# Optimization experiments

Measured on AMD Instinct MI355X. Metric: run time of the kernel, lower is better.

Reference implementation:

```python
import jax, jax.numpy as jnp
import numpy as np

EMBED_DIM = 1024
NUM_HEADS = 16
HEAD_DIM = EMBED_DIM // NUM_HEADS
B, N = 4, 2048


def setup_inputs() -> dict:
    key = jax.random.key(0)
    k = jax.random.split(key, 5)
    scale = 1.0 / np.sqrt(EMBED_DIM)
    return {
        "x": jax.random.normal(k[0], (B, N, EMBED_DIM), dtype=jnp.float32),
        # torch nn.Linear convention: y = x @ W.T + b, W shape [out, in]
        "qkv_w": jax.random.uniform(k[1], (3 * EMBED_DIM, EMBED_DIM), jnp.float32, -scale, scale),
        "qkv_b": jax.random.uniform(k[2], (3 * EMBED_DIM,), jnp.float32, -scale, scale),
        "out_w": jax.random.uniform(k[3], (EMBED_DIM, EMBED_DIM), jnp.float32, -scale, scale),
        "out_b": jax.random.uniform(k[4], (EMBED_DIM,), jnp.float32, -scale, scale),
    }


def reference(x, qkv_w, qkv_b, out_w, out_b):
    b, n, e = x.shape
    qkv = x @ qkv_w.T + qkv_b                      # [B,N,3E]
    qkv = qkv.reshape(b, n, 3, NUM_HEADS, HEAD_DIM)
    qkv = jnp.transpose(qkv, (2, 0, 3, 1, 4))      # [3,B,H,N,D]
    q, k, v = qkv[0], qkv[1], qkv[2]
    scores = jnp.einsum("bhqd,bhkd->bhqk", q, k) / np.sqrt(HEAD_DIM)
    weights = jax.nn.softmax(scores, axis=-1)
    attn = jnp.einsum("bhqk,bhkd->bhqd", weights, v)  # [B,H,N,D]
    attn = jnp.transpose(attn, (0, 2, 1, 3)).reshape(b, n, e)
    return attn @ out_w.T + out_b
```

## Files before the change

### kernel.cpp

```cpp
#include <hip/hip_runtime.h>
#include <hip/hip_bf16.h>

#define EMBED 1024
#define NHEADS 16
#define HDIM 64
#define BATCH 4
#define SEQ 2048
#define MROWS (BATCH*SEQ)
#define QKVN (3*EMBED)
#define KDIM 1024

typedef __bf16 bf16;
typedef __bf16 bf16x4 __attribute__((ext_vector_type(4)));
typedef __bf16 bf16x8 __attribute__((ext_vector_type(8)));
typedef float f32x4 __attribute__((ext_vector_type(4)));
typedef float f32x16 __attribute__((ext_vector_type(16)));

#define QSCALE 0.18033688011112042f

#define NX (MROWS*EMBED/4)
#define NQ (QKVN*KDIM/4)
#define NO (EMBED*KDIM/4)
__global__ void cvt_all(const float* __restrict__ x, const float* __restrict__ qw,
                        const float* __restrict__ ow,
                        bf16* __restrict__ xb, bf16* __restrict__ qwb, bf16* __restrict__ owb) {
    int i = blockIdx.x * blockDim.x + threadIdx.x;
    const float* src; bf16* dst; int j;
    if (i < NX)            { src = x;  dst = xb;  j = i; }
    else if (i < NX + NQ)  { src = qw; dst = qwb; j = i - NX; }
    else if (i < NX+NQ+NO) { src = ow; dst = owb; j = i - NX - NQ; }
    else return;
    float4 f = ((const float4*)src)[j];
    bf16x4 o;
    o[0] = (bf16)f.x; o[1] = (bf16)f.y; o[2] = (bf16)f.z; o[3] = (bf16)f.w;
    *((bf16x4*)dst + j) = o;
}

template<int MODE>
__launch_bounds__(256)
__global__ void gemm_bt(const bf16* __restrict__ A, const bf16* __restrict__ B,
                        const float* __restrict__ bias,
                        float* __restrict__ outF,
                        bf16* __restrict__ Qb, bf16* __restrict__ Kb, bf16* __restrict__ Vt)
{
    __shared__ bf16 Alds[128][32];
    __shared__ bf16 Blds[128][32];
    const int tid = threadIdx.x;
    const int l = tid & 63, w = tid >> 6;
    const int wr = w >> 1, wc = w & 1;
    const int tM = blockIdx.y * 128, tN = blockIdx.x * 128;

    f32x4 acc[4][4] = {};
    const bf16* Abase = A + (size_t)tM * KDIM;
    const bf16* Bbase = B + (size_t)tN * KDIM;

    for (int k0 = 0; k0 < KDIM; k0 += 32) {
        #pragma unroll
        for (int t = 0; t < 2; ++t) {
            int idx = t * 256 + tid;
            int row = idx >> 2;
            int kc = (idx & 3) * 8;
            __builtin_amdgcn_global_load_lds(
                (const __attribute__((address_space(1))) void*)(Abase + (size_t)row * KDIM + k0 + kc),
                (__attribute__((address_space(3))) void*)((char*)&Alds[0][0] + idx * 16),
                16, 0, 0);
            __builtin_amdgcn_global_load_lds(
                (const __attribute__((address_space(1))) void*)(Bbase + (size_t)row * KDIM + k0 + kc),
                (__attribute__((address_space(3))) void*)((char*)&Blds[0][0] + idx * 16),
                16, 0, 0);
        }
        __syncthreads();
        bf16x8 a[4], b[4];
        #pragma unroll
        for (int i = 0; i < 4; ++i)
            a[i] = *(const bf16x8*)&Alds[wr * 64 + i * 16 + (l & 15)][(l >> 4) * 8];
        #pragma unroll
        for (int j = 0; j < 4; ++j)
            b[j] = *(const bf16x8*)&Blds[wc * 64 + j * 16 + (l & 15)][(l >> 4) * 8];
        #pragma unroll
        for (int i = 0; i < 4; ++i)
            #pragma unroll
            for (int j = 0; j < 4; ++j)
                acc[i][j] = __builtin_amdgcn_mfma_f32_16x16x32_bf16(a[i], b[j], acc[i][j], 0, 0, 0);
        __syncthreads();
    }

    #pragma unroll
    for (int i = 0; i < 4; ++i) {
        #pragma unroll
        for (int j = 0; j < 4; ++j) {
            int n = tN + wc * 64 + j * 16 + (l & 15);
            float bv = bias[n];
            #pragma unroll
            for (int r = 0; r < 4; ++r) {
                int m = tM + wr * 64 + i * 16 + (l >> 4) * 4 + r;
                float v = acc[i][j][r] + bv;
                if (MODE == 1) {
                    outF[(size_t)m * EMBED + n] = v;
                } else {
                    int which = n >> 10, nn = n & 1023;
                    int hd = nn >> 6, d = nn & 63;
                    int bidx = m >> 11, ns = m & 2047;
                    int bh = bidx * NHEADS + hd;
                    int t32 = ns >> 5;
                    if (which == 2) {
                        int rem16 = ns & 15;
                        int c = (ns >> 4) & 1;
                        int fj = (rem16 & 3) | ((rem16 & 8) >> 1);
                        int fhi = (rem16 >> 2) & 1;
                        int dblk = d >> 5;
                        int lane = (d & 31) | (fhi << 5);
                        size_t idx = ((((size_t)bh * 64 + t32) * 2 + dblk) * 2 + c) * 512 + lane * 8 + fj;
                        Vt[idx] = (bf16)v;
                    } else {
                        int kk = d >> 4, fhi = (d >> 3) & 1, fj = d & 7;
                        int lane = (ns & 31) | (fhi << 5);
                        size_t idx = (((size_t)bh * 64 + t32) * 4 + kk) * 512 + lane * 8 + fj;
                        if (which == 0) Qb[idx] = (bf16)(v * QSCALE);
                        else            Kb[idx] = (bf16)v;
                    }
                }
            }
        }
    }
}

static __device__ __forceinline__ unsigned cvt_pk(float lo, float hi) {
    unsigned r;
    asm("v_cvt_pk_bf16_f32 %0, %1, %2" : "=v"(r) : "v"(lo), "v"(hi));
    return r;
}

__launch_bounds__(256)
__global__ void attn_kernel(const bf16* __restrict__ Qb, const bf16* __restrict__ Kb,
                            const bf16* __restrict__ Vt, bf16* __restrict__ AO)
{
    const int tid = threadIdx.x, l = tid & 63, w = tid >> 6;
    const int lo5 = l & 31, hi = l >> 5;
    int bid = blockIdx.x;
    int swz = (bid & 7) * 128 + (bid >> 3);
    const int bh = swz >> 4;
    const int qt = swz & 15;

    const bf16* QFh = Qb + (size_t)bh * (64 * 2048);
    const bf16* Kit = Kb + (size_t)bh * (64 * 2048) + (size_t)l * 8;
    const bf16* Vit = Vt + (size_t)bh * (64 * 2048) + (size_t)l * 8;

    const int qtile = qt * 4 + w;
    const bf16* qbase = QFh + (size_t)qtile * 2048 + (size_t)l * 8;
    bf16x8 qf[4];
    #pragma unroll
    for (int kk = 0; kk < 4; ++kk)
        qf[kk] = *(const bf16x8*)(qbase + kk * 512);

    f32x16 O0 = {}, O1 = {};
    float lsum = 0.f;

    bf16x8 kK0, kK1, kK2, kK3;
    kK0 = *(const bf16x8*)(Kit);
    kK1 = *(const bf16x8*)(Kit + 512);
    kK2 = *(const bf16x8*)(Kit + 1024);
    kK3 = *(const bf16x8*)(Kit + 1536);
    f32x16 SA, SB;
    #pragma unroll
    for (int r = 0; r < 16; ++r) SA[r] = 0.f;
    SA = __builtin_amdgcn_mfma_f32_32x32x16_bf16(kK0, qf[0], SA, 0, 0, 0);
    SA = __builtin_amdgcn_mfma_f32_32x32x16_bf16(kK1, qf[1], SA, 0, 0, 0);
    SA = __builtin_amdgcn_mfma_f32_32x32x16_bf16(kK2, qf[2], SA, 0, 0, 0);
    SA = __builtin_amdgcn_mfma_f32_32x32x16_bf16(kK3, qf[3], SA, 0, 0, 0);
    kK0 = *(const bf16x8*)(Kit + 2048);
    kK1 = *(const bf16x8*)(Kit + 2048 + 512);
    kK2 = *(const bf16x8*)(Kit + 2048 + 1024);
    kK3 = *(const bf16x8*)(Kit + 2048 + 1536);

#define ATTN_BODY(T, SCUR, SNXT)                                                        \
    {                                                                                    \
        const int t = (T);                                                               \
        const bf16* vb = Vit + (size_t)t * 2048;                                         \
        bf16x8 vf00 = *(const bf16x8*)(vb);                                              \
        bf16x8 vf01 = *(const bf16x8*)(vb + 512);                                        \
        bf16x8 vf10 = *(const bf16x8*)(vb + 1024);                                       \
        bf16x8 vf11 = *(const bf16x8*)(vb + 1536);                                       \
        __builtin_amdgcn_s_setprio(1);                                                   \
        _Pragma("unroll")                                                                \
        for (int r = 0; r < 16; ++r) SNXT[r] = 0.f;                                      \
        SNXT = __builtin_amdgcn_mfma_f32_32x32x16_bf16(kK0, qf[0], SNXT, 0, 0, 0);       \
        SNXT = __builtin_amdgcn_mfma_f32_32x32x16_bf16(kK1, qf[1], SNXT, 0, 0, 0);       \
        SNXT = __builtin_amdgcn_mfma_f32_32x32x16_bf16(kK2, qf[2], SNXT, 0, 0, 0);       \
        SNXT = __builtin_amdgcn_mfma_f32_32x32x16_bf16(kK3, qf[3], SNXT, 0, 0, 0);       \
        __builtin_amdgcn_s_setprio(0);                                                   \
        int tp = t + 2; tp = (tp < 64) ? tp : 0;                                         \
        const bf16* kb = Kit + (size_t)tp * 2048;                                        \
        kK0 = *(const bf16x8*)(kb);                                                      \
        kK1 = *(const bf16x8*)(kb + 512);                                                \
        kK2 = *(const bf16x8*)(kb + 1024);                                               \
        kK3 = *(const bf16x8*)(kb + 1536);                                               \
        float p[16];                                                                     \
        _Pragma("unroll")                                                                \
        for (int r = 0; r < 16; ++r)                                                     \
            p[r] = __builtin_amdgcn_exp2f(SCUR[r]);                                      \
        float s0 = (p[0] + p[1]) + (p[2] + p[3]);                                        \
        float s1 = (p[4] + p[5]) + (p[6] + p[7]);                                        \
        float s2 = (p[8] + p[9]) + (p[10] + p[11]);                                      \
        float s3 = (p[12] + p[13]) + (p[14] + p[15]);                                    \
        lsum += (s0 + s1) + (s2 + s3);                                                   \
        union { unsigned u[4]; bf16x8 v; } pk0, pk1;                                     \
        pk0.u[0] = cvt_pk(p[0], p[1]);   pk0.u[1] = cvt_pk(p[2], p[3]);                  \
        pk0.u[2] = cvt_pk(p[4], p[5]);   pk0.u[3] = cvt_pk(p[6], p[7]);                  \
        pk1.u[0] = cvt_pk(p[8], p[9]);   pk1.u[1] = cvt_pk(p[10], p[11]);                \
        pk1.u[2] = cvt_pk(p[12], p[13]); pk1.u[3] = cvt_pk(p[14], p[15]);                \
        __builtin_amdgcn_s_setprio(1);                                                   \
        O0 = __builtin_amdgcn_mfma_f32_32x32x16_bf16(vf00, pk0.v, O0, 0, 0, 0);          \
        O0 = __builtin_amdgcn_mfma_f32_32x32x16_bf16(vf01, pk1.v, O0, 0, 0, 0);          \
        O1 = __builtin_amdgcn_mfma_f32_32x32x16_bf16(vf10, pk0.v, O1, 0, 0, 0);          \
        O1 = __builtin_amdgcn_mfma_f32_32x32x16_bf16(vf11, pk1.v, O1, 0, 0, 0);          \
        __builtin_amdgcn_s_setprio(0);                                                   \
    }

    for (int t2 = 0; t2 < 64; t2 += 2) {
        ATTN_BODY(t2,     SA, SB)
        ATTN_BODY(t2 + 1, SB, SA)
    }
#undef ATTN_BODY

    lsum += __shfl_xor(lsum, 32);
    float linv = 1.0f / lsum;

    const int b = bh >> 4, hd = bh & 15;
    const int q0 = qt * 128 + w * 32;
    bf16* outp = &AO[(size_t)(b * SEQ + q0 + lo5) * EMBED + hd * HDIM];
    #pragma unroll
    for (int g = 0; g < 4; ++g) {
        bf16x4 o0, o1;
        #pragma unroll
        for (int r4 = 0; r4 < 4; ++r4) {
            o0[r4] = (bf16)(O0[g * 4 + r4] * linv);
            o1[r4] = (bf16)(O1[g * 4 + r4] * linv);
        }
        *(bf16x4*)&outp[g * 8 + hi * 4] = o0;
        *(bf16x4*)&outp[32 + g * 8 + hi * 4] = o1;
    }
}

extern "C" void kernel_launch(void* const* d_in, const int* in_sizes, int n_in,
                              void* d_out, int out_size, void* d_ws, size_t ws_size,
                              hipStream_t stream) {
    const float* x     = (const float*)d_in[0];
    const float* qkv_w = (const float*)d_in[1];
    const float* qkv_b = (const float*)d_in[2];
    const float* out_w = (const float*)d_in[3];
    const float* out_b = (const float*)d_in[4];
    float* out = (float*)d_out;

    char* ws = (char*)d_ws;
    bf16* xb  = (bf16*)(ws);
    bf16* qwb = (bf16*)(ws + 16777216);
    bf16* owb = (bf16*)(ws + 23068672);
    bf16* Qb  = (bf16*)(ws + 25165824);
    bf16* Kb  = (bf16*)(ws + 41943040);
    bf16* Vt  = (bf16*)(ws + 58720256);
    bf16* AO  = (bf16*)(ws + 75497472);

    cvt_all<<<(NX + NQ + NO + 255) / 256, 256, 0, stream>>>(x, qkv_w, out_w, xb, qwb, owb);

    gemm_bt<0><<<dim3(QKVN / 128, MROWS / 128), 256, 0, stream>>>(
        xb, qwb, qkv_b, nullptr, Qb, Kb, Vt);

    attn_kernel<<<BATCH * NHEADS * (SEQ / 128), 256, 0, stream>>>(Qb, Kb, Vt, AO);

    gemm_bt<1><<<dim3(EMBED / 128, MROWS / 128), 256, 0, stream>>>(
        AO, owb, out_b, out, nullptr, nullptr, nullptr);
}
```

Baseline: 201.7 us.

## Stage QKV epilogue through LDS for coalesced stores and prefetch V a tile ahead

The QKV GEMM epilogue used to scatter single bf16 values straight to global memory in the attention fragment layout. It now writes the biased, scaled values into an LDS bounce buffer that reuses the GEMM tile space, in two passes, then copies them out as contiguous 16-byte stores. The attention kernel now also double-buffers V fragments in registers, loading the next tile's V one iteration early so the load latency overlaps the current compute. The costs are extra barriers and LDS traffic in the epilogue and more registers in the attention loop, which could lower occupancy.

New measurement: 200.7 us. Within noise of the previous version (-0.5%).

```diff
diff --git a/kernel.cpp b/kernel.cpp
--- a/kernel.cpp
+++ b/kernel.cpp
@@ -43,8 +43,11 @@
                         float* __restrict__ outF,
                         bf16* __restrict__ Qb, bf16* __restrict__ Kb, bf16* __restrict__ Vt)
 {
-    __shared__ bf16 Alds[128][32];
-    __shared__ bf16 Blds[128][32];
+    __shared__ __align__(16) char ldsmem[16384];
+    bf16 (*Alds)[32] = (bf16(*)[32])ldsmem;
+    bf16 (*Blds)[32] = (bf16(*)[32])(ldsmem + 8192);
+    bf16* bounce = (bf16*)ldsmem;
+
     const int tid = threadIdx.x;
     const int l = tid & 63, w = tid >> 6;
     const int wr = w >> 1, wc = w & 1;
@@ -85,41 +88,72 @@
         __syncthreads();
     }
 
-    #pragma unroll
-    for (int i = 0; i < 4; ++i) {
-        #pragma unroll
-        for (int j = 0; j < 4; ++j) {
-            int n = tN + wc * 64 + j * 16 + (l & 15);
-            float bv = bias[n];
+    if (MODE == 1) {
+        #pragma unroll
+        for (int i = 0; i < 4; ++i) {
             #pragma unroll
-            for (int r = 0; r < 4; ++r) {
-                int m = tM + wr * 64 + i * 16 + (l >> 4) * 4 + r;
-                float v = acc[i][j][r] + bv;
-                if (MODE == 1) {
-                    outF[(size_t)m * EMBED + n] = v;
-                } else {
-                    int which = n >> 10, nn = n & 1023;
-                    int hd = nn >> 6, d = nn & 63;
-                    int bidx = m >> 11, ns = m & 2047;
-                    int bh = bidx * NHEADS + hd;
-                    int t32 = ns >> 5;
-                    if (which == 2) {
-                        int rem16 = ns & 15;
-                        int c = (ns >> 4) & 1;
-                        int fj = (rem16 & 3) | ((rem16 & 8) >> 1);
-                        int fhi = (rem16 >> 2) & 1;
-                        int dblk = d >> 5;
-                        int lane = (d & 31) | (fhi << 5);
-                        size_t idx = ((((size_t)bh * 64 + t32) * 2 + dblk) * 2 + c) * 512 + lane * 8 + fj;
-                        Vt[idx] = (bf16)v;
-                    } else {
-                        int kk = d >> 4, fhi = (d >> 3) & 1, fj = d & 7;
-                        int lane = (ns & 31) | (fhi << 5);
-                        size_t idx = (((size_t)bh * 64 + t32) * 4 + kk) * 512 + lane * 8 + fj;
-                        if (which == 0) Qb[idx] = (bf16)(v * QSCALE);
-                        else            Kb[idx] = (bf16)v;
+            for (int j = 0; j < 4; ++j) {
+                int n = tN + wc * 64 + j * 16 + (l & 15);
+                float bv = bias[n];
+                #pragma unroll
+                for (int r = 0; r < 4; ++r) {
+                    int m = tM + wr * 64 + i * 16 + (l >> 4) * 4 + r;
+                    outF[(size_t)m * EMBED + n] = acc[i][j][r] + bv;
+                }
+            }
+        }
+    } else {
+        const int which = tN >> 10;
+        const int bidx  = tM >> 11;
+        const int hd0   = (tN & 1023) >> 6;
+        const int t32base = (tM & 2047) >> 5;
+        bf16* dstbase = (which == 0) ? Qb : (which == 1) ? Kb : Vt;
+        const float scale = (which == 0) ? QSCALE : 1.0f;
+
+        float bj[4];
+        #pragma unroll
+        for (int j = 0; j < 4; ++j)
+            bj[j] = bias[tN + wc * 64 + j * 16 + (l & 15)];
+
+        #pragma unroll
+        for (int pass = 0; pass < 2; ++pass) {
+            __syncthreads();
+            #pragma unroll
+            for (int ii = 0; ii < 2; ++ii) {
+                const int i = pass * 2 + ii;
+                #pragma unroll
+                for (int j = 0; j < 4; ++j) {
+                    const int d = (wc * 64 + j * 16 + (l & 15)) & 63;
+                    #pragma unroll
+                    for (int r = 0; r < 4; ++r) {
+                        const int nsl = wr * 64 + i * 16 + (l >> 4) * 4 + r;
+                        float v = acc[i][j][r] + bj[j];
+                        int off;
+                        if (which == 2) {
+                            int dblk = d >> 5;
+                            int rem16 = nsl & 15;
+                            int c = (nsl >> 4) & 1;
+                            int fj = (rem16 & 3) | ((rem16 & 8) >> 1);
+                            int fhi = (rem16 >> 2) & 1;
+                            int lane = (d & 31) | (fhi << 5);
+                            off = (dblk * 2 + c) * 512 + lane * 8 + fj;
+                        } else {
+                            int kk = d >> 4, fhi = (d >> 3) & 1, fj = d & 7;
+                            int lane = (nsl & 31) | (fhi << 5);
+                            off = kk * 512 + lane * 8 + fj;
+                        }
+                        bounce[(wc * 2 + wr) * 2048 + off] = (bf16)(v * scale);
                     }
                 }
+            }
+            __syncthreads();
+            const int chunk = tid >> 6;
+            size_t gbase = ((size_t)(bidx * NHEADS + hd0 + (chunk >> 1)) * 64
+                            + t32base + 2 * (chunk & 1) + pass) * 2048;
+            #pragma unroll
+            for (int s = 0; s < 4; ++s) {
+                int eoff = s * 512 + (tid & 63) * 8;
+                *(bf16x8*)(dstbase + gbase + eoff) = *(const bf16x8*)&bounce[chunk * 2048 + eoff];
             }
         }
     }
@@ -156,11 +190,17 @@
     f32x16 O0 = {}, O1 = {};
     float lsum = 0.f;
 
-    bf16x8 kK0, kK1, kK2, kK3;
-    kK0 = *(const bf16x8*)(Kit);
-    kK1 = *(const bf16x8*)(Kit + 512);
-    kK2 = *(const bf16x8*)(Kit + 1024);
-    kK3 = *(const bf16x8*)(Kit + 1536);
+    bf16x8 vA00 = *(const bf16x8*)(Vit);
+    bf16x8 vA01 = *(const bf16x8*)(Vit + 512);
+    bf16x8 vA10 = *(const bf16x8*)(Vit + 1024);
+    bf16x8 vA11 = *(const bf16x8*)(Vit + 1536);
+    bf16x8 vB00, vB01, vB10, vB11;
+
+    bf16x8 kK0 = *(const bf16x8*)(Kit);
+    bf16x8 kK1 = *(const bf16x8*)(Kit + 512);
+    bf16x8 kK2 = *(const bf16x8*)(Kit + 1024);
+    bf16x8 kK3 = *(const bf16x8*)(Kit + 1536);
+
     f32x16 SA, SB;
     #pragma unroll
     for (int r = 0; r < 16; ++r) SA[r] = 0.f;
@@ -173,14 +213,15 @@
     kK2 = *(const bf16x8*)(Kit + 2048 + 1024);
     kK3 = *(const bf16x8*)(Kit + 2048 + 1536);
 
-#define ATTN_BODY(T, SCUR, SNXT)                                                        \
+#define ATTN_BODY(T, SCUR, SNXT, VC00, VC01, VC10, VC11, VN00, VN01, VN10, VN11)        \
     {                                                                                    \
         const int t = (T);                                                               \
-        const bf16* vb = Vit + (size_t)t * 2048;                                         \
-        bf16x8 vf00 = *(const bf16x8*)(vb);                                              \
-        bf16x8 vf01 = *(const bf16x8*)(vb + 512);                                        \
-        bf16x8 vf10 = *(const bf16x8*)(vb + 1024);                                       \
-        bf16x8 vf11 = *(const bf16x8*)(vb + 1536);                                       \
+        int tv = t + 1; tv = (tv < 64) ? tv : 0;                                         \
+        const bf16* vb = Vit + (size_t)tv * 2048;                                        \
+        VN00 = *(const bf16x8*)(vb);                                                     \
+        VN01 = *(const bf16x8*)(vb + 512);                                               \
+        VN10 = *(const bf16x8*)(vb + 1024);                                              \
+        VN11 = *(const bf16x8*)(vb + 1536);                                              \
         __builtin_amdgcn_s_setprio(1);                                                   \
         _Pragma("unroll")                                                                \
         for (int r = 0; r < 16; ++r) SNXT[r] = 0.f;                                      \
@@ -210,16 +251,16 @@
         pk1.u[0] = cvt_pk(p[8], p[9]);   pk1.u[1] = cvt_pk(p[10], p[11]);                \
         pk1.u[2] = cvt_pk(p[12], p[13]); pk1.u[3] = cvt_pk(p[14], p[15]);                \
         __builtin_amdgcn_s_setprio(1);                                                   \
-        O0 = __builtin_amdgcn_mfma_f32_32x32x16_bf16(vf00, pk0.v, O0, 0, 0, 0);          \
-        O0 = __builtin_amdgcn_mfma_f32_32x32x16_bf16(vf01, pk1.v, O0, 0, 0, 0);          \
-        O1 = __builtin_amdgcn_mfma_f32_32x32x16_bf16(vf10, pk0.v, O1, 0, 0, 0);          \
-        O1 = __builtin_amdgcn_mfma_f32_32x32x16_bf16(vf11, pk1.v, O1, 0, 0, 0);          \
+        O0 = __builtin_amdgcn_mfma_f32_32x32x16_bf16(VC00, pk0.v, O0, 0, 0, 0);          \
+        O0 = __builtin_amdgcn_mfma_f32_32x32x16_bf16(VC01, pk1.v, O0, 0, 0, 0);          \
+        O1 = __builtin_amdgcn_mfma_f32_32x32x16_bf16(VC10, pk0.v, O1, 0, 0, 0);          \
+        O1 = __builtin_amdgcn_mfma_f32_32x32x16_bf16(VC11, pk1.v, O1, 0, 0, 0);          \
         __builtin_amdgcn_s_setprio(0);                                                   \
     }
 
     for (int t2 = 0; t2 < 64; t2 += 2) {
-        ATTN_BODY(t2,     SA, SB)
-        ATTN_BODY(t2 + 1, SB, SA)
+        ATTN_BODY(t2,     SA, SB, vA00, vA01, vA10, vA11, vB00, vB01, vB10, vB11)
+        ATTN_BODY(t2 + 1, SB, SA, vB00, vB01, vB10, vB11, vA00, vA01, vA10, vA11)
     }
 #undef ATTN_BODY
 
```
